# Performance work log

Hardware: AMD Instinct MI355X
Metric: run time of the kernel (lower is better)

## Reference

```python
import jax, jax.numpy as jnp
import numpy as np

IN_CHN = 8192
OUT_CHN = 8192
BATCH = 64


def setup_inputs() -> dict:
    key = jax.random.key(0)
    kx, kw = jax.random.split(key)
    x = jax.random.normal(kx, (BATCH, IN_CHN), dtype=jnp.float32)
    # mirrors torch.rand(shape) * 0.001 (uniform in [0, 0.001))
    weight = jax.random.uniform(kw, (OUT_CHN, IN_CHN), dtype=jnp.float32) * 0.001
    return {"x": x, "weight": weight}


def reference(x, weight):
    # Training-path forward of HardBinary (STE binarization):
    # forward value is scale * sign(W); gradient flows through clamp(W, -1, 1).
    scale = jax.lax.stop_gradient(jnp.mean(jnp.abs(weight)))
    binary = scale * jnp.sign(weight)
    clipped = jnp.clip(weight, -1.0, 1.0)
    w = jax.lax.stop_gradient(binary - clipped) + clipped  # value == binary
    # F.linear(x, w) == x @ w.T ; [B, in] @ [in, out] -> [B, out]
    return jnp.einsum("bi,oi->bo", x, w)
```

## Files before the change

### kernel.cpp

```cpp
#include <hip/hip_runtime.h>

#define K_DIM 8192
#define N_DIM 8192
#define M_DIM 64

typedef __attribute__((ext_vector_type(8))) short bf16x8;
typedef __attribute__((ext_vector_type(4))) float fx4;

#define NTILE 64
#define KSPLIT 4
#define KBLK (K_DIM / KSPLIT)
#define KCHUNK (KBLK / 4)

__device__ __forceinline__ short bf16_rne(float f) {
    unsigned u = __builtin_bit_cast(unsigned, f);
    u += 0x7FFFu + ((u >> 16) & 1u);
    return (short)(u >> 16);
}

__global__ void hb_xconv(const float* __restrict__ x, short* __restrict__ xb) {
    const int i = blockIdx.x * blockDim.x + threadIdx.x;
    const fx4* xp = reinterpret_cast<const fx4*>(x) + (size_t)i * 2;
    fx4 a = xp[0], b = xp[1];
    bf16x8 o;
    #pragma unroll
    for (int j = 0; j < 4; ++j) { o[j] = bf16_rne(a[j]); o[j + 4] = bf16_rne(b[j]); }
    reinterpret_cast<bf16x8*>(xb)[i] = o;
}

template<bool XBF16>
__global__ __launch_bounds__(256, 2)
void hb_gemm(const float* __restrict__ x, const float* __restrict__ w,
             const short* __restrict__ xb, float* __restrict__ out,
             float* __restrict__ absacc)
{
    __shared__ float red[4][M_DIM][NTILE];
    const int tid  = threadIdx.x;
    const int wid  = tid >> 6;
    const int lane = tid & 63;
    const int lr   = lane & 15;
    const int lg   = lane >> 4;

    const int nblk  = blockIdx.x & 127;
    const int kblk  = blockIdx.x >> 7;
    const int nbase = nblk * NTILE;
    const int kbase = kblk * KBLK + wid * KCHUNK;

    fx4 acc[4][4] = {};
    float wabs = 0.f;

    #pragma unroll 2
    for (int ks = 0; ks < KCHUNK; ks += 32) {
        const int kpos = kbase + ks + lg * 8;

        bf16x8 afrag[4];
        #pragma unroll
        for (int mt = 0; mt < 4; ++mt) {
            const int b = mt * 16 + lr;
            if constexpr (XBF16) {
                afrag[mt] = *reinterpret_cast<const bf16x8*>(xb + (size_t)b * K_DIM + kpos);
            } else {
                const float* xp = x + (size_t)b * K_DIM + kpos;
                fx4 a0 = *reinterpret_cast<const fx4*>(xp);
                fx4 a1 = *reinterpret_cast<const fx4*>(xp + 4);
                bf16x8 f;
                #pragma unroll
                for (int j = 0; j < 4; ++j) { f[j] = bf16_rne(a0[j]); f[j + 4] = bf16_rne(a1[j]); }
                afrag[mt] = f;
            }
        }

        bf16x8 bfrag[4];
        #pragma unroll
        for (int nt = 0; nt < 4; ++nt) {
            const float* wp = w + (size_t)(nbase + nt * 16 + lr) * K_DIM + kpos;
            fx4 w0 = *reinterpret_cast<const fx4*>(wp);
            fx4 w1 = *reinterpret_cast<const fx4*>(wp + 4);
            bf16x8 s;
            #pragma unroll
            for (int j = 0; j < 4; ++j) {
                const float v0 = w0[j], v1 = w1[j];
                wabs += fabsf(v0) + fabsf(v1);
                s[j]     = (v0 > 0.f) ? (short)0x3F80 : ((v0 < 0.f) ? (short)0xBF80 : (short)0);
                s[j + 4] = (v1 > 0.f) ? (short)0x3F80 : ((v1 < 0.f) ? (short)0xBF80 : (short)0);
            }
            bfrag[nt] = s;
        }

        #pragma unroll
        for (int mt = 0; mt < 4; ++mt)
            #pragma unroll
            for (int nt = 0; nt < 4; ++nt)
                acc[mt][nt] = __builtin_amdgcn_mfma_f32_16x16x32_bf16(
                    afrag[mt], bfrag[nt], acc[mt][nt], 0, 0, 0);
    }

    #pragma unroll
    for (int off = 32; off > 0; off >>= 1)
        wabs += __shfl_down(wabs, off);
    if (lane == 0) atomicAdd(absacc, wabs);

    #pragma unroll
    for (int mt = 0; mt < 4; ++mt)
        #pragma unroll
        for (int nt = 0; nt < 4; ++nt)
            #pragma unroll
            for (int j = 0; j < 4; ++j)
                red[wid][mt * 16 + lg * 4 + j][nt * 16 + lr] = acc[mt][nt][j];
    __syncthreads();

    #pragma unroll
    for (int e = 0; e < 16; ++e) {
        const int p = e * 256 + tid;
        const int m = p >> 6;
        const int n = p & 63;
        const float s = red[0][m][n] + red[1][m][n] + red[2][m][n] + red[3][m][n];
        atomicAdd(out + (size_t)m * N_DIM + nbase + n, s);
    }
}

__global__ void hb_scale(float* __restrict__ out, const float* __restrict__ absacc) {
    const float scale = absacc[0] * (1.0f / ((float)K_DIM * (float)N_DIM));
    const int i = blockIdx.x * blockDim.x + threadIdx.x;
    fx4* p = reinterpret_cast<fx4*>(out);
    fx4 v = p[i];
    v *= scale;
    p[i] = v;
}

extern "C" void kernel_launch(void* const* d_in, const int* in_sizes, int n_in,
                              void* d_out, int out_size, void* d_ws, size_t ws_size,
                              hipStream_t stream) {
    const float* x = (const float*)d_in[0];
    const float* w = (const float*)d_in[1];
    float* out = (float*)d_out;

    float* absacc = (float*)d_ws;
    short* xb = (short*)((char*)d_ws + 256);
    const size_t xb_bytes = (size_t)M_DIM * K_DIM * sizeof(short);
    const bool use_xb = ws_size >= 256 + xb_bytes;

    hipMemsetAsync(d_out, 0, (size_t)out_size * sizeof(float), stream);
    hipMemsetAsync(d_ws, 0, 64, stream);

    if (use_xb) {
        hb_xconv<<<256, 256, 0, stream>>>(x, xb);
        hb_gemm<true><<<(N_DIM / NTILE) * KSPLIT, 256, 0, stream>>>(x, w, xb, out, absacc);
    } else {
        hb_gemm<false><<<(N_DIM / NTILE) * KSPLIT, 256, 0, stream>>>(x, w, nullptr, out, absacc);
    }
    hb_scale<<<512, 256, 0, stream>>>(out, absacc);
}
```

Baseline: 389.8 us.

## Split K sixteen ways into partial buffers, reduce and scale in final pass

Each wave now handles its own 16-column strip over a K slice of 512 instead of four waves sharing a 64-column tile over K/4. The LDS reduction and the atomicAdds into the output are gone. Partial sums go to a workspace buffer per K split, and a reduce kernel sums them and applies the scale. This raises the block count to 2048 with higher occupancy, so the weight stream should be spread more evenly and the atomic contention and output memset are removed. The cost is extra traffic for 16 partial buffers of 2 MB each, and it assumes the workspace is large enough with no fallback.

Result: slower. 475.0 us (+21.9%).

```diff
diff --git a/kernel.cpp b/kernel.cpp
--- a/kernel.cpp
+++ b/kernel.cpp
@@ -3,14 +3,11 @@
 #define K_DIM 8192
 #define N_DIM 8192
 #define M_DIM 64
+#define KSPLIT 16
+#define KBLK (K_DIM / KSPLIT)
 
 typedef __attribute__((ext_vector_type(8))) short bf16x8;
 typedef __attribute__((ext_vector_type(4))) float fx4;
-
-#define NTILE 64
-#define KSPLIT 4
-#define KBLK (K_DIM / KSPLIT)
-#define KCHUNK (KBLK / 4)
 
 __device__ __forceinline__ short bf16_rne(float f) {
     unsigned u = __builtin_bit_cast(unsigned, f);
@@ -28,71 +25,49 @@
     reinterpret_cast<bf16x8*>(xb)[i] = o;
 }
 
-template<bool XBF16>
-__global__ __launch_bounds__(256, 2)
-void hb_gemm(const float* __restrict__ x, const float* __restrict__ w,
-             const short* __restrict__ xb, float* __restrict__ out,
-             float* __restrict__ absacc)
+__global__ __launch_bounds__(256, 6)
+void hb_gemm(const float* __restrict__ w, const short* __restrict__ xb,
+             float* __restrict__ part, float* __restrict__ absacc)
 {
-    __shared__ float red[4][M_DIM][NTILE];
     const int tid  = threadIdx.x;
     const int wid  = tid >> 6;
     const int lane = tid & 63;
     const int lr   = lane & 15;
     const int lg   = lane >> 4;
 
-    const int nblk  = blockIdx.x & 127;
-    const int kblk  = blockIdx.x >> 7;
-    const int nbase = nblk * NTILE;
-    const int kbase = kblk * KBLK + wid * KCHUNK;
+    const int kblk  = blockIdx.x & (KSPLIT - 1);
+    const int nbase = (blockIdx.x >> 4) * 64 + wid * 16;
+    const int kbase = kblk * KBLK;
 
-    fx4 acc[4][4] = {};
+    const float* wp = w  + (size_t)(nbase + lr) * K_DIM + kbase + lg * 8;
+    const short* xp = xb + (size_t)lr * K_DIM + kbase + lg * 8;
+
+    fx4 acc[4] = {};
     float wabs = 0.f;
 
     #pragma unroll 2
-    for (int ks = 0; ks < KCHUNK; ks += 32) {
-        const int kpos = kbase + ks + lg * 8;
+    for (int ks = 0; ks < KBLK; ks += 32) {
+        const fx4 w0 = *reinterpret_cast<const fx4*>(wp + ks);
+        const fx4 w1 = *reinterpret_cast<const fx4*>(wp + ks + 4);
 
         bf16x8 afrag[4];
         #pragma unroll
-        for (int mt = 0; mt < 4; ++mt) {
-            const int b = mt * 16 + lr;
-            if constexpr (XBF16) {
-                afrag[mt] = *reinterpret_cast<const bf16x8*>(xb + (size_t)b * K_DIM + kpos);
-            } else {
-                const float* xp = x + (size_t)b * K_DIM + kpos;
-                fx4 a0 = *reinterpret_cast<const fx4*>(xp);
-                fx4 a1 = *reinterpret_cast<const fx4*>(xp + 4);
-                bf16x8 f;
-                #pragma unroll
-                for (int j = 0; j < 4; ++j) { f[j] = bf16_rne(a0[j]); f[j + 4] = bf16_rne(a1[j]); }
-                afrag[mt] = f;
-            }
-        }
+        for (int mt = 0; mt < 4; ++mt)
+            afrag[mt] = *reinterpret_cast<const bf16x8*>(xp + (size_t)mt * 16 * K_DIM + ks);
 
-        bf16x8 bfrag[4];
+        bf16x8 bfrag;
         #pragma unroll
-        for (int nt = 0; nt < 4; ++nt) {
-            const float* wp = w + (size_t)(nbase + nt * 16 + lr) * K_DIM + kpos;
-            fx4 w0 = *reinterpret_cast<const fx4*>(wp);
-            fx4 w1 = *reinterpret_cast<const fx4*>(wp + 4);
-            bf16x8 s;
-            #pragma unroll
-            for (int j = 0; j < 4; ++j) {
-                const float v0 = w0[j], v1 = w1[j];
-                wabs += fabsf(v0) + fabsf(v1);
-                s[j]     = (v0 > 0.f) ? (short)0x3F80 : ((v0 < 0.f) ? (short)0xBF80 : (short)0);
-                s[j + 4] = (v1 > 0.f) ? (short)0x3F80 : ((v1 < 0.f) ? (short)0xBF80 : (short)0);
-            }
-            bfrag[nt] = s;
+        for (int j = 0; j < 4; ++j) {
+            const float v0 = w0[j], v1 = w1[j];
+            wabs += fabsf(v0);
+            wabs += fabsf(v1);
+            bfrag[j]     = (v0 > 0.f) ? (short)0x3F80 : ((v0 < 0.f) ? (short)0xBF80 : (short)0);
+            bfrag[j + 4] = (v1 > 0.f) ? (short)0x3F80 : ((v1 < 0.f) ? (short)0xBF80 : (short)0);
         }
 
         #pragma unroll
         for (int mt = 0; mt < 4; ++mt)
-            #pragma unroll
-            for (int nt = 0; nt < 4; ++nt)
-                acc[mt][nt] = __builtin_amdgcn_mfma_f32_16x16x32_bf16(
-                    afrag[mt], bfrag[nt], acc[mt][nt], 0, 0, 0);
+            acc[mt] = __builtin_amdgcn_mfma_f32_16x16x32_bf16(afrag[mt], bfrag, acc[mt], 0, 0, 0);
     }
 
     #pragma unroll
@@ -100,32 +75,25 @@
         wabs += __shfl_down(wabs, off);
     if (lane == 0) atomicAdd(absacc, wabs);
 
+    float* pp = part + (size_t)kblk * (M_DIM * N_DIM) + nbase + lr;
     #pragma unroll
     for (int mt = 0; mt < 4; ++mt)
         #pragma unroll
-        for (int nt = 0; nt < 4; ++nt)
-            #pragma unroll
-            for (int j = 0; j < 4; ++j)
-                red[wid][mt * 16 + lg * 4 + j][nt * 16 + lr] = acc[mt][nt][j];
-    __syncthreads();
-
-    #pragma unroll
-    for (int e = 0; e < 16; ++e) {
-        const int p = e * 256 + tid;
-        const int m = p >> 6;
-        const int n = p & 63;
-        const float s = red[0][m][n] + red[1][m][n] + red[2][m][n] + red[3][m][n];
-        atomicAdd(out + (size_t)m * N_DIM + nbase + n, s);
-    }
+        for (int j = 0; j < 4; ++j)
+            pp[(size_t)(mt * 16 + lg * 4 + j) * N_DIM] = acc[mt][j];
 }
 
-__global__ void hb_scale(float* __restrict__ out, const float* __restrict__ absacc) {
-    const float scale = absacc[0] * (1.0f / ((float)K_DIM * (float)N_DIM));
+__global__ void hb_reduce(const float* __restrict__ part,
+                          const float* __restrict__ absacc,
+                          float* __restrict__ out) {
+    const float scale = absacc[0] * (1.0f / 67108864.0f);
     const int i = blockIdx.x * blockDim.x + threadIdx.x;
-    fx4* p = reinterpret_cast<fx4*>(out);
-    fx4 v = p[i];
-    v *= scale;
-    p[i] = v;
+    fx4 s = reinterpret_cast<const fx4*>(part)[i];
+    #pragma unroll
+    for (int k = 1; k < KSPLIT; ++k)
+        s += reinterpret_cast<const fx4*>(part)[(size_t)k * (M_DIM * N_DIM / 4) + i];
+    s *= scale;
+    reinterpret_cast<fx4*>(out)[i] = s;
 }
 
 extern "C" void kernel_launch(void* const* d_in, const int* in_sizes, int n_in,
@@ -136,18 +104,11 @@
     float* out = (float*)d_out;
 
     float* absacc = (float*)d_ws;
-    short* xb = (short*)((char*)d_ws + 256);
-    const size_t xb_bytes = (size_t)M_DIM * K_DIM * sizeof(short);
-    const bool use_xb = ws_size >= 256 + xb_bytes;
+    short* xb     = (short*)((char*)d_ws + 4096);
+    float* part   = (float*)((char*)d_ws + (2u << 20));
 
-    hipMemsetAsync(d_out, 0, (size_t)out_size * sizeof(float), stream);
     hipMemsetAsync(d_ws, 0, 64, stream);
-
-    if (use_xb) {
-        hb_xconv<<<256, 256, 0, stream>>>(x, xb);
-        hb_gemm<true><<<(N_DIM / NTILE) * KSPLIT, 256, 0, stream>>>(x, w, xb, out, absacc);
-    } else {
-        hb_gemm<false><<<(N_DIM / NTILE) * KSPLIT, 256, 0, stream>>>(x, w, nullptr, out, absacc);
-    }
-    hb_scale<<<512, 256, 0, stream>>>(out, absacc);
+    hb_xconv<<<256, 256, 0, stream>>>(x, xb);
+    hb_gemm<<<(N_DIM / 64) * KSPLIT, 256, 0, stream>>>(w, xb, part, absacc);
+    hb_reduce<<<512, 256, 0, stream>>>(part, absacc, out);
 }
```
